# Kernel tuning notes

Hardware: AMD Instinct MI355X
Metric: run time of the kernel (lower is better)

Reference implementation:

```python
import jax, jax.numpy as jnp
import numpy as np

B, T, E, NH = 2, 2048, 512, 8
HD = E // NH
SCALE = float(HD) ** -0.5


def setup_inputs() -> dict:
    key = jax.random.key(0)
    ks = jax.random.split(key, 7)
    s = 0.02
    return {
        "x": jax.random.normal(ks[0], (B, T, E), dtype=jnp.float32),
        "w_qkv": jax.random.normal(ks[1], (E, 3 * E), dtype=jnp.float32) * s,
        "b_qkv": jax.random.normal(ks[2], (3 * E,), dtype=jnp.float32) * s,
        "w_od": jax.random.normal(ks[3], (E, 2 * NH), dtype=jnp.float32) * s,
        "b_od": jax.random.normal(ks[4], (2 * NH,), dtype=jnp.float32) * s,
        "w_out": jax.random.normal(ks[5], (E, E), dtype=jnp.float32) * s,
        "b_out": jax.random.normal(ks[6], (E,), dtype=jnp.float32) * s,
    }


def _heads(t):  # (B,T,E) -> (B*NH, T, HD)
    return t.reshape(B, T, NH, HD).transpose(0, 2, 1, 3).reshape(B * NH, T, HD)


def _point_mask(idx, j):  # idx: (B*NH,T) float indices -> one-hot (B*NH,T,T)
    return (j[None, None, :] == idx[:, :, None]).astype(jnp.float32)


def reference(x, w_qkv, b_qkv, w_od, b_od, w_out, b_out):
    qkv = x @ w_qkv + b_qkv
    Q, K, V = jnp.split(qkv, 3, axis=-1)  # each (B,T,E)

    od = Q @ w_od + b_od  # (B,T,2*NH)
    offset, duration = jnp.split(od, 2, axis=-1)
    offset = jnp.tanh(offset) * T
    duration = jax.nn.sigmoid(duration) * T

    query_index = jnp.arange(T, dtype=x.dtype)[None, :, None]  # (1,T,1)
    anchor = query_index + offset  # (B,T,NH)
    # 'b t nh -> (b nh) t'
    anchor = anchor.transpose(0, 2, 1).reshape(B * NH, T)
    duration = duration.transpose(0, 2, 1).reshape(B * NH, T)

    start = anchor - duration
    end = anchor + duration
    bound_l = jnp.floor(start)
    bound_r = jnp.ceil(end)
    anchor_l = jnp.floor(anchor)
    anchor_r = anchor_l + 1.0

    j = jnp.arange(T, dtype=x.dtype)
    neg_bound_weight = (bound_l - start)[:, :, None] * _point_mask(bound_l, j) \
                     + (end - bound_r)[:, :, None] * _point_mask(bound_r, j)
    anchor_dist_l = anchor - anchor_l
    anchor_weight = anchor_dist_l[:, :, None] * _point_mask(anchor_r, j) \
                  + (1.0 - anchor_dist_l)[:, :, None] * _point_mask(anchor_l, j)
    point_weight = 1.0 + neg_bound_weight + anchor_weight  # (B*NH,T,T)

    # segment mask: True OUTSIDE [bound_l, bound_r]
    attn_mask = (j[None, None, :] < bound_l[:, :, None]) | (j[None, None, :] > bound_r[:, :, None])

    Qh, Kh, Vh = _heads(Q), _heads(K), _heads(V)  # (B*NH, T, HD)
    scores = jnp.einsum('bic,brc->bir', Qh, Kh) * SCALE * point_weight
    scores = jnp.where(attn_mask, jnp.asarray(-1e8, scores.dtype), scores)
    attn = jax.nn.softmax(scores, axis=-1)
    out = jnp.einsum('bir,brc->bic', attn, Vh)  # (B*NH,T,HD)
    out = out.reshape(B, NH, T, HD).transpose(0, 2, 1, 3).reshape(B, T, E)
    return out @ w_out + b_out
```

## Files before the change

kernel.cpp:

```cpp
#include <hip/hip_runtime.h>
#include <math.h>

typedef float vf4 __attribute__((ext_vector_type(4)));
typedef float f32x4 __attribute__((ext_vector_type(4)));
typedef short bf16x8 __attribute__((ext_vector_type(8)));
typedef short short4v __attribute__((ext_vector_type(4)));
typedef int int2v __attribute__((ext_vector_type(2)));

constexpr int B = 2, T = 2048, E = 512, NH = 8, HD = 64;
constexpr int BH = B * NH;
constexpr int NT = BH * T;
constexpr float SCALE = 0.125f;

static __device__ __forceinline__ short f2bf(float f) {
  unsigned u = __float_as_uint(f);
  unsigned r = (u + 0x7fffu + ((u >> 16) & 1u)) >> 16;
  return (short)r;
}
static __device__ __forceinline__ unsigned pk2bf(float a, float b) {
  unsigned lo = (unsigned)(unsigned short)f2bf(a);
  unsigned hi = (unsigned)(unsigned short)f2bf(b);
  return lo | (hi << 16);
}

__global__ __launch_bounds__(256) void cast_x_bf16(
    const float* __restrict__ x, short* __restrict__ xb)
{
  int idx = (blockIdx.x * 256 + threadIdx.x) * 4;
  vf4 v = *(const vf4*)&x[idx];
  short4v o;
  o[0] = f2bf(v[0]); o[1] = f2bf(v[1]); o[2] = f2bf(v[2]); o[3] = f2bf(v[3]);
  *(short4v*)&xb[idx] = o;
}

__global__ __launch_bounds__(256) void cast_w_T(
    const float* __restrict__ w, short* __restrict__ wT, int N)
{
  __shared__ float t[32][33];
  const int k0 = blockIdx.x * 32;
  const int n0 = blockIdx.y * 32;
  const int c = threadIdx.x & 31, r = threadIdx.x >> 5;
#pragma unroll
  for (int p = 0; p < 4; ++p)
    t[r + p * 8][c] = w[(size_t)(k0 + r + p * 8) * N + n0 + c];
  __syncthreads();
#pragma unroll
  for (int p = 0; p < 4; ++p)
    wT[(size_t)(n0 + r + p * 8) * 512 + k0 + c] = f2bf(t[c][r + p * 8]);
}

__global__ __launch_bounds__(256) void w_comb(
    const float* __restrict__ w_qkv, const float* __restrict__ b_qkv,
    const float* __restrict__ w_od, const float* __restrict__ b_od,
    float* __restrict__ Wc, float* __restrict__ bc)
{
  __shared__ float Lod[512 * 16];
  __shared__ float pb[16][17];
  const int tid = threadIdx.x;
#pragma unroll
  for (int p = 0; p < 8; ++p) {
    int idx = (p * 256 + tid) * 4;
    *(vf4*)&Lod[idx] = *(const vf4*)&w_od[idx];
  }
  __syncthreads();

  if (blockIdx.x < 32) {
    const int k = blockIdx.x * 16 + (tid >> 4);
    const int c = tid & 15;
    float s = 0.0f;
    for (int m = 0; m < E; m += 4) {
      vf4 wq = *(const vf4*)&w_qkv[(size_t)k * 1536 + m];
      s += wq[0] * Lod[(m + 0) * 16 + c] + wq[1] * Lod[(m + 1) * 16 + c]
         + wq[2] * Lod[(m + 2) * 16 + c] + wq[3] * Lod[(m + 3) * 16 + c];
    }
    Wc[k * 16 + c] = s;
  } else {
    const int c = tid & 15, seg = tid >> 4;
    float s = 0.0f;
    for (int m = seg * 32; m < seg * 32 + 32; ++m)
      s += b_qkv[m] * Lod[m * 16 + c];
    pb[seg][c] = s;
    __syncthreads();
    if (tid < 16) {
      float acc = b_od[tid];
#pragma unroll
      for (int g = 0; g < 16; ++g) acc += pb[g][tid];
      bc[tid] = acc;
    }
  }
}

__global__ __launch_bounds__(256) void qkv_gemm_bf16(
    const short* __restrict__ xb, const short* __restrict__ wT,
    const float* __restrict__ bias, short* __restrict__ qkvb)
{
  __shared__ __align__(16) short As[128 * 40];
  __shared__ __align__(16) short Bt[128 * 40];

  const int tid = threadIdx.x;
  const int wave = tid >> 6, lane = tid & 63;
  const int quad = lane >> 4, l15 = lane & 15;
  const int wm = wave >> 1, wn = wave & 1;
  const int m0 = blockIdx.y * 128, n0 = blockIdx.x * 128;

  f32x4 acc[4][4];
#pragma unroll
  for (int mi = 0; mi < 4; ++mi)
#pragma unroll
    for (int ni = 0; ni < 4; ++ni) acc[mi][ni] = (f32x4){0, 0, 0, 0};

  const int sr = tid >> 1, sc = (tid & 1) * 16;

#pragma unroll 1
  for (int k0 = 0; k0 < E; k0 += 32) {
    __syncthreads();
    *(bf16x8*)&As[sr * 40 + sc] =
        *(const bf16x8*)&xb[(size_t)(m0 + sr) * 512 + k0 + sc];
    *(bf16x8*)&As[sr * 40 + sc + 8] =
        *(const bf16x8*)&xb[(size_t)(m0 + sr) * 512 + k0 + sc + 8];
    *(bf16x8*)&Bt[sr * 40 + sc] =
        *(const bf16x8*)&wT[(size_t)(n0 + sr) * 512 + k0 + sc];
    *(bf16x8*)&Bt[sr * 40 + sc + 8] =
        *(const bf16x8*)&wT[(size_t)(n0 + sr) * 512 + k0 + sc + 8];
    __syncthreads();

    bf16x8 aA[4], bB[4];
#pragma unroll
    for (int mi = 0; mi < 4; ++mi)
      aA[mi] = *(const bf16x8*)&As[(wm * 64 + mi * 16 + l15) * 40 + quad * 8];
#pragma unroll
    for (int ni = 0; ni < 4; ++ni)
      bB[ni] = *(const bf16x8*)&Bt[(wn * 64 + ni * 16 + l15) * 40 + quad * 8];
#pragma unroll
    for (int mi = 0; mi < 4; ++mi)
#pragma unroll
      for (int ni = 0; ni < 4; ++ni)
        acc[mi][ni] = __builtin_amdgcn_mfma_f32_16x16x32_bf16(
            aA[mi], bB[ni], acc[mi][ni], 0, 0, 0);
  }

#pragma unroll
  for (int mi = 0; mi < 4; ++mi)
#pragma unroll
    for (int ni = 0; ni < 4; ++ni)
#pragma unroll
      for (int r = 0; r < 4; ++r) {
        int row = m0 + wm * 64 + mi * 16 + quad * 4 + r;
        int col = n0 + wn * 64 + ni * 16 + l15;
        float v = acc[mi][ni][r] + bias[col];
        if (col < 512) v *= SCALE;
        qkvb[(size_t)row * 1536 + col] = f2bf(v);
      }
}

__global__ __launch_bounds__(256) void od_params(
    const float* __restrict__ x, const float* __restrict__ Wc,
    const float* __restrict__ bc, float* __restrict__ prm)
{
  __shared__ float od_s[16][16];
  const int tid = threadIdx.x;
  const int r = tid >> 4, c = tid & 15;
  const int row = blockIdx.x * 16 + r;

  float sum = bc[c];
  const float* qr = x + (size_t)row * E;
  for (int k = 0; k < E; k += 4) {
    vf4 q = *(const vf4*)&qr[k];
    sum += q[0] * Wc[(k + 0) * 16 + c]
         + q[1] * Wc[(k + 1) * 16 + c]
         + q[2] * Wc[(k + 2) * 16 + c]
         + q[3] * Wc[(k + 3) * 16 + c];
  }
  od_s[r][c] = sum;
  __syncthreads();

  if (tid < 128) {
    const int rr = tid >> 3, h = tid & 7;
    const int grow = blockIdx.x * 16 + rr;
    const int b = grow / T, i = grow % T;
    float o = od_s[rr][h];
    float d = od_s[rr][h + 8];
    float offset   = tanhf(o) * (float)T;
    float duration = (float)T / (1.0f + expf(-d));
    float anchor = (float)i + offset;
    float start = anchor - duration;
    float end   = anchor + duration;
    float bl = floorf(start);
    float br = ceilf(end);
    float al = floorf(anchor);
    float wbl = bl - start;
    float wbr = end - br;
    float af  = anchor - al;
    float rsc = 1.0f;
    if (br < 0.0f || bl > (float)(T - 1)) {
      bl = 0.0f; br = (float)(T - 1);
      wbl = 0.0f; wbr = 0.0f; al = -5.0f; af = 0.0f;
      rsc = 0.0f;
    }
    int idx = (b * NH + h) * T + i;
    prm[0 * NT + idx] = bl;
    prm[1 * NT + idx] = br;
    prm[2 * NT + idx] = wbl;
    prm[3 * NT + idx] = wbr;
    prm[4 * NT + idx] = al;
    prm[5 * NT + idx] = af;
    prm[6 * NT + idx] = rsc;
  }
}

__global__ __launch_bounds__(256) void v_transpose(
    const short* __restrict__ qkvb, short* __restrict__ Vtg)
{
  __shared__ __align__(16) short Tt[64 * 72];
  const int tid = threadIdx.x;
  const int t0 = blockIdx.x * 64, bh = blockIdx.y;
  const int b = bh >> 3, h = bh & 7;
  const int rq = tid >> 3, cb = (tid & 7) * 8;
#pragma unroll
  for (int it = 0; it < 2; ++it) {
    int rr = it * 32 + rq;
    bf16x8 v = *(const bf16x8*)&qkvb[(size_t)(b * T + t0 + rr) * 1536 + 1024 + h * 64 + cb];
#pragma unroll
    for (int j = 0; j < 8; ++j) Tt[(cb + j) * 72 + rr] = v[j];
  }
  __syncthreads();
  const int hd = tid >> 2, tc = (tid & 3) * 16;
  *(bf16x8*)&Vtg[(size_t)(bh * 64 + hd) * T + t0 + tc] =
      *(const bf16x8*)&Tt[hd * 72 + tc];
  *(bf16x8*)&Vtg[(size_t)(bh * 64 + hd) * T + t0 + tc + 8] =
      *(const bf16x8*)&Tt[hd * 72 + tc + 8];
}

__global__ __launch_bounds__(256, 4) void flash_attn_mfma3(
    const short* __restrict__ qkvb, const short* __restrict__ Vtg,
    const float* __restrict__ prm,
    float* __restrict__ Opart, float* __restrict__ lpart)
{
  __shared__ __align__(16) short Ks[64 * 72];
  __shared__ __align__(16) short Vt[64 * 72];
  __shared__ __align__(16) short Ps[4][16 * 72];
  __shared__ float u_s[8];

  const int tid = threadIdx.x;
  const int wave = tid >> 6, lane = tid & 63;
  const int quad = lane >> 4, l15 = lane & 15;
  const int qt = blockIdx.x, bh = blockIdx.y, ks = blockIdx.z;
  const int b = bh >> 3, h = bh & 7;
  const int i0 = qt * 64;
  const int i = i0 + wave * 16 + l15;

  const int pidx = bh * T + i;
  float blf = prm[0 * NT + pidx];
  float brf = prm[1 * NT + pidx];
  float wbl = prm[2 * NT + pidx];
  float wbr = prm[3 * NT + pidx];
  float alf = prm[4 * NT + pidx];
  float afr = prm[5 * NT + pidx];
  float rsc = prm[6 * NT + pidx];
  const int bli = (int)blf, widi = (int)brf - bli, ali = (int)alf;
  const unsigned widu = (unsigned)widi;
  const float a1 = 1.0f - afr;

  bf16x8 aQ0, aQ1;
  {
    size_t bq = (size_t)(b * T + i) * 1536 + h * 64;
    aQ0 = *(const bf16x8*)&qkvb[bq + quad * 8];
    aQ1 = *(const bf16x8*)&qkvb[bq + 32 + quad * 8];
    if (rsc == 0.0f) {
      bf16x8 z = {0, 0, 0, 0, 0, 0, 0, 0};
      aQ0 = z; aQ1 = z;
    }
  }

  float bmn = blf, bmx = brf;
#pragma unroll
  for (int d = 1; d < 64; d <<= 1) {
    bmn = fminf(bmn, __shfl_xor(bmn, d));
    bmx = fmaxf(bmx, __shfl_xor(bmx, d));
  }
  if (lane == 0) { u_s[wave * 2] = bmn; u_s[wave * 2 + 1] = bmx; }
  __syncthreads();
  bmn = fminf(fminf(u_s[0], u_s[2]), fminf(u_s[4], u_s[6]));
  bmx = fmaxf(fmaxf(u_s[1], u_s[3]), fmaxf(u_s[5], u_s[7]));
  const int ktlo = max(ks * 16, max(((int)bmn) >> 6, 0));
  const int kthi = min(ks * 16 + 15, min(((int)bmx) >> 6, T / 64 - 1));

  f32x4 o[4];
#pragma unroll
  for (int c = 0; c < 4; ++c) o[c] = (f32x4){0, 0, 0, 0};
  float lacc = 0.0f;

  const int rq = tid >> 3, cb = (tid & 7) * 8;

#pragma unroll 1
  for (int kt = ktlo; kt <= kthi; ++kt) {
    const int j0 = kt * 64;
    __syncthreads();
#pragma unroll
    for (int it = 0; it < 2; ++it) {
      int rr = it * 32 + rq;
      *(bf16x8*)&Ks[rr * 72 + cb] =
          *(const bf16x8*)&qkvb[(size_t)(b * T + j0 + rr) * 1536 + 512 + h * 64 + cb];
      *(bf16x8*)&Vt[rr * 72 + cb] =
          *(const bf16x8*)&Vtg[(size_t)(bh * 64 + rr) * T + j0 + cb];
    }
    __syncthreads();

    f32x4 s[4];
#pragma unroll
    for (int nc = 0; nc < 4; ++nc) {
      const short* kb = &Ks[(nc * 16 + l15) * 72 + quad * 8];
      f32x4 a = (f32x4){0, 0, 0, 0};
      a = __builtin_amdgcn_mfma_f32_16x16x32_bf16(*(const bf16x8*)&kb[0],  aQ0, a, 0, 0, 0);
      a = __builtin_amdgcn_mfma_f32_16x16x32_bf16(*(const bf16x8*)&kb[32], aQ1, a, 0, 0, 0);
      s[nc] = a;
    }

    const int dq  = j0 + quad * 4 - bli;
    const int dq2 = j0 + quad * 4 - ali;
#pragma unroll
    for (int nc = 0; nc < 4; ++nc) {
      const int dn = dq + nc * 16, d2n = dq2 + nc * 16;
      float pr[4];
#pragma unroll
      for (int r = 0; r < 4; ++r) {
        int d = dn + r, d2 = d2n + r;
        float e  = (d == 0) ? wbl : ((d == widi) ? wbr : 0.0f);
        float aw = (d2 == 0) ? a1 : ((d2 == 1) ? afr : 0.0f);
        float w = 1.0f + e + aw;
        float v = s[nc][r] * w;
        v = ((unsigned)d <= widu) ? v : -80.0f;
        float p = __expf(v);
        lacc += p;
        pr[r] = p;
      }
      int2v pk;
      pk[0] = (int)pk2bf(pr[0], pr[1]);
      pk[1] = (int)pk2bf(pr[2], pr[3]);
      *(int2v*)&Ps[wave][l15 * 72 + nc * 16 + quad * 4] = pk;
    }

    bf16x8 bP0 = *(const bf16x8*)&Ps[wave][l15 * 72 + quad * 8];
    bf16x8 bP1 = *(const bf16x8*)&Ps[wave][l15 * 72 + 32 + quad * 8];
#pragma unroll
    for (int nc2 = 0; nc2 < 4; ++nc2) {
      const short* vb = &Vt[(nc2 * 16 + l15) * 72 + quad * 8];
      o[nc2] = __builtin_amdgcn_mfma_f32_16x16x32_bf16(
          *(const bf16x8*)&vb[0],  bP0, o[nc2], 0, 0, 0);
      o[nc2] = __builtin_amdgcn_mfma_f32_16x16x32_bf16(
          *(const bf16x8*)&vb[32], bP1, o[nc2], 0, 0, 0);
    }
  }

  lacc += __shfl_xor(lacc, 16);
  lacc += __shfl_xor(lacc, 32);
  if (lane < 16)
    lpart[ks * NT + bh * T + i] = lacc;

  size_t ob = (size_t)ks * (B * T * E) + (size_t)(b * T + i) * E + h * 64;
#pragma unroll
  for (int nc2 = 0; nc2 < 4; ++nc2)
    *(f32x4*)&Opart[ob + nc2 * 16 + quad * 4] = o[nc2];
}

__global__ __launch_bounds__(256) void combine_attn(
    const float* __restrict__ Opart, const float* __restrict__ lpart,
    short* __restrict__ attnb)
{
  int base = (blockIdx.x * 256 + threadIdx.x) * 4;
  int row = base >> 9;
  int c = base & 511;
  int h = c >> 6;
  int b = row >> 11;
  int i = row & (T - 1);
  int lidx = ((b << 3) + h) * T + i;
  float l = lpart[lidx] + lpart[NT + lidx];
  float inv = 1.0f / l;
  vf4 o0 = *(const vf4*)&Opart[base];
  vf4 o1 = *(const vf4*)&Opart[(size_t)(B * T * E) + base];
  short4v ov;
#pragma unroll
  for (int j = 0; j < 4; ++j) ov[j] = f2bf((o0[j] + o1[j]) * inv);
  *(short4v*)&attnb[base] = ov;
}

__global__ __launch_bounds__(256) void out_gemm_bf16(
    const short* __restrict__ Ab, const short* __restrict__ wT,
    const float* __restrict__ bias, float* __restrict__ Co)
{
  __shared__ __align__(16) short As[64 * 40];
  __shared__ __align__(16) short Bt[64 * 40];

  const int tid = threadIdx.x;
  const int wave = tid >> 6, lane = tid & 63;
  const int quad = lane >> 4, l15 = lane & 15;
  const int wm = wave >> 1, wn = wave & 1;
  const int m0 = blockIdx.y * 64, n0 = blockIdx.x * 64;

  f32x4 acc[2][2];
#pragma unroll
  for (int mi = 0; mi < 2; ++mi)
#pragma unroll
    for (int ni = 0; ni < 2; ++ni) acc[mi][ni] = (f32x4){0, 0, 0, 0};

  const int ar = tid >> 2, akc = (tid & 3) * 8;

#pragma unroll 1
  for (int k0 = 0; k0 < E; k0 += 32) {
    __syncthreads();
    *(bf16x8*)&As[ar * 40 + akc] =
        *(const bf16x8*)&Ab[(size_t)(m0 + ar) * 512 + k0 + akc];
    *(bf16x8*)&Bt[ar * 40 + akc] =
        *(const bf16x8*)&wT[(size_t)(n0 + ar) * 512 + k0 + akc];
    __syncthreads();

    bf16x8 aA[2], bB[2];
#pragma unroll
    for (int mi = 0; mi < 2; ++mi)
      aA[mi] = *(const bf16x8*)&As[(wm * 32 + mi * 16 + l15) * 40 + quad * 8];
#pragma unroll
    for (int ni = 0; ni < 2; ++ni)
      bB[ni] = *(const bf16x8*)&Bt[(wn * 32 + ni * 16 + l15) * 40 + quad * 8];
#pragma unroll
    for (int mi = 0; mi < 2; ++mi)
#pragma unroll
      for (int ni = 0; ni < 2; ++ni)
        acc[mi][ni] = __builtin_amdgcn_mfma_f32_16x16x32_bf16(
            aA[mi], bB[ni], acc[mi][ni], 0, 0, 0);
  }

#pragma unroll
  for (int mi = 0; mi < 2; ++mi)
#pragma unroll
    for (int ni = 0; ni < 2; ++ni)
#pragma unroll
      for (int r = 0; r < 4; ++r) {
        int row = m0 + wm * 32 + mi * 16 + quad * 4 + r;
        int col = n0 + wn * 32 + ni * 16 + l15;
        Co[(size_t)row * 512 + col] = acc[mi][ni][r] + bias[col];
      }
}

extern "C" void kernel_launch(void* const* d_in, const int* in_sizes, int n_in,
                              void* d_out, int out_size, void* d_ws, size_t ws_size,
                              hipStream_t stream)
{
  const float* x     = (const float*)d_in[0];
  const float* w_qkv = (const float*)d_in[1];
  const float* b_qkv = (const float*)d_in[2];
  const float* w_od  = (const float*)d_in[3];
  const float* b_od  = (const float*)d_in[4];
  const float* w_out = (const float*)d_in[5];
  const float* b_out = (const float*)d_in[6];
  float* out = (float*)d_out;

  char* w = (char*)d_ws;
  short* xb    = (short*)w;  w += (size_t)B * T * E * 2;
  short* wTq   = (short*)w;  w += (size_t)E * 3 * E * 2;
  short* wTo   = (short*)w;  w += (size_t)E * E * 2;
  short* qkvb  = (short*)w;  w += (size_t)B * T * 3 * E * 2;
  float* Wc    = (float*)w;  w += (size_t)E * 16 * 4;
  float* bc    = (float*)w;  w += 256;
  float* prm   = (float*)w;  w += (size_t)7 * NT * 4;
  float* Opart = (float*)w;  w += (size_t)2 * B * T * E * 4;
  float* lpart = (float*)w;  w += (size_t)2 * NT * 4;
  short* attnb = (short*)w;  w += (size_t)B * T * E * 2;
  short* Vtg   = xb;

  cast_x_bf16<<<dim3(B * T * E / 1024), 256, 0, stream>>>(x, xb);
  cast_w_T<<<dim3(E / 32, 3 * E / 32), 256, 0, stream>>>(w_qkv, wTq, 3 * E);
  cast_w_T<<<dim3(E / 32, E / 32), 256, 0, stream>>>(w_out, wTo, E);
  w_comb<<<dim3(33), 256, 0, stream>>>(w_qkv, b_qkv, w_od, b_od, Wc, bc);

  qkv_gemm_bf16<<<dim3(3 * E / 128, B * T / 128), 256, 0, stream>>>(
      xb, wTq, b_qkv, qkvb);

  od_params<<<dim3(B * T / 16), 256, 0, stream>>>(x, Wc, bc, prm);

  v_transpose<<<dim3(T / 64, BH), 256, 0, stream>>>(qkvb, Vtg);

  flash_attn_mfma3<<<dim3(T / 64, BH, 2), 256, 0, stream>>>(
      qkvb, Vtg, prm, Opart, lpart);

  combine_attn<<<dim3(B * T * E / 1024), 256, 0, stream>>>(Opart, lpart, attnb);

  out_gemm_bf16<<<dim3(E / 64, B * T / 64), 256, 0, stream>>>(
      attnb, wTo, b_out, out);
}
```

Baseline: 197.8 us.

## Fuse prep kernels, write V transposed from QKV GEMM, fast-path attention softmax

Merges the x cast, the two weight transposes and the od-weight combine into one prep launch. The QKV GEMM epilogue now writes V directly in transposed layout, which removes the separate transpose kernel. Q is prescaled by log2e so attention can use exp2, with a wave-uniform fast path that skips the point-weight and mask logic on tiles that touch no boundary or anchor. Attention partial outputs are stored as bf16 to halve combine traffic, and the out-projection GEMM tile is widened to 128 columns. The bf16 partials and truncation-style packing of P reduce precision somewhat.

Result: faster. 183.2 us (-7.4%).

```diff
diff --git a/kernel.cpp b/kernel.cpp
--- a/kernel.cpp
+++ b/kernel.cpp
@@ -6,11 +6,14 @@
 typedef short bf16x8 __attribute__((ext_vector_type(8)));
 typedef short short4v __attribute__((ext_vector_type(4)));
 typedef int int2v __attribute__((ext_vector_type(2)));
+typedef int int4v __attribute__((ext_vector_type(4)));
 
 constexpr int B = 2, T = 2048, E = 512, NH = 8, HD = 64;
 constexpr int BH = B * NH;
 constexpr int NT = BH * T;
 constexpr float SCALE = 0.125f;
+constexpr float LOG2E = 1.44269504088896f;
+constexpr float QSC = SCALE * LOG2E;
 
 static __device__ __forceinline__ short f2bf(float f) {
   unsigned u = __float_as_uint(f);
@@ -22,77 +25,94 @@
   unsigned hi = (unsigned)(unsigned short)f2bf(b);
   return lo | (hi << 16);
 }
-
-__global__ __launch_bounds__(256) void cast_x_bf16(
-    const float* __restrict__ x, short* __restrict__ xb)
-{
-  int idx = (blockIdx.x * 256 + threadIdx.x) * 4;
-  vf4 v = *(const vf4*)&x[idx];
-  short4v o;
-  o[0] = f2bf(v[0]); o[1] = f2bf(v[1]); o[2] = f2bf(v[2]); o[3] = f2bf(v[3]);
-  *(short4v*)&xb[idx] = o;
-}
-
-__global__ __launch_bounds__(256) void cast_w_T(
-    const float* __restrict__ w, short* __restrict__ wT, int N)
-{
-  __shared__ float t[32][33];
-  const int k0 = blockIdx.x * 32;
-  const int n0 = blockIdx.y * 32;
-  const int c = threadIdx.x & 31, r = threadIdx.x >> 5;
-#pragma unroll
-  for (int p = 0; p < 4; ++p)
-    t[r + p * 8][c] = w[(size_t)(k0 + r + p * 8) * N + n0 + c];
-  __syncthreads();
-#pragma unroll
-  for (int p = 0; p < 4; ++p)
-    wT[(size_t)(n0 + r + p * 8) * 512 + k0 + c] = f2bf(t[c][r + p * 8]);
-}
-
-__global__ __launch_bounds__(256) void w_comb(
-    const float* __restrict__ w_qkv, const float* __restrict__ b_qkv,
-    const float* __restrict__ w_od, const float* __restrict__ b_od,
-    float* __restrict__ Wc, float* __restrict__ bc)
-{
-  __shared__ float Lod[512 * 16];
-  __shared__ float pb[16][17];
+static __device__ __forceinline__ unsigned pkhu(float a, float b) {
+  unsigned ua = __float_as_uint(a) + 0x8000u;
+  unsigned ub = __float_as_uint(b) + 0x8000u;
+  return __builtin_amdgcn_perm(ub, ua, 0x07060302u);
+}
+#if __has_builtin(__builtin_amdgcn_exp2f)
+#define EXP2F(x) __builtin_amdgcn_exp2f(x)
+#else
+#define EXP2F(x) exp2f(x)
+#endif
+static __device__ __forceinline__ float bf2f(short s) {
+  return __uint_as_float(((unsigned)(unsigned short)s) << 16);
+}
+
+__global__ __launch_bounds__(256) void prep_all(
+    const float* __restrict__ x, const float* __restrict__ w_qkv,
+    const float* __restrict__ b_qkv, const float* __restrict__ w_od,
+    const float* __restrict__ b_od,
+    short* __restrict__ xb, short* __restrict__ wTq, short* __restrict__ wTo,
+    const float* __restrict__ w_out, float* __restrict__ Wc,
+    float* __restrict__ bc)
+{
+  __shared__ float sh[8464];
+  const int bid = blockIdx.x;
   const int tid = threadIdx.x;
-#pragma unroll
-  for (int p = 0; p < 8; ++p) {
-    int idx = (p * 256 + tid) * 4;
-    *(vf4*)&Lod[idx] = *(const vf4*)&w_od[idx];
-  }
-  __syncthreads();
-
-  if (blockIdx.x < 32) {
-    const int k = blockIdx.x * 16 + (tid >> 4);
-    const int c = tid & 15;
-    float s = 0.0f;
-    for (int m = 0; m < E; m += 4) {
-      vf4 wq = *(const vf4*)&w_qkv[(size_t)k * 1536 + m];
-      s += wq[0] * Lod[(m + 0) * 16 + c] + wq[1] * Lod[(m + 1) * 16 + c]
-         + wq[2] * Lod[(m + 2) * 16 + c] + wq[3] * Lod[(m + 3) * 16 + c];
-    }
-    Wc[k * 16 + c] = s;
+
+  if (bid < 2048) {
+    int idx = (bid * 256 + tid) * 4;
+    vf4 v = *(const vf4*)&x[idx];
+    short4v o;
+    o[0] = f2bf(v[0]); o[1] = f2bf(v[1]); o[2] = f2bf(v[2]); o[3] = f2bf(v[3]);
+    *(short4v*)&xb[idx] = o;
+  } else if (bid < 3072) {
+    const float* w; short* wT; int N, t;
+    if (bid < 2816) { t = bid - 2048; w = w_qkv; wT = wTq; N = 1536; }
+    else            { t = bid - 2816; w = w_out; wT = wTo; N = 512; }
+    float (*tt)[33] = (float(*)[33])sh;
+    const int k0 = (t & 15) * 32;
+    const int n0 = (t >> 4) * 32;
+    const int c = tid & 31, r = tid >> 5;
+#pragma unroll
+    for (int p = 0; p < 4; ++p)
+      tt[r + p * 8][c] = w[(size_t)(k0 + r + p * 8) * N + n0 + c];
+    __syncthreads();
+#pragma unroll
+    for (int p = 0; p < 4; ++p)
+      wT[(size_t)(n0 + r + p * 8) * 512 + k0 + c] = f2bf(tt[c][r + p * 8]);
   } else {
-    const int c = tid & 15, seg = tid >> 4;
-    float s = 0.0f;
-    for (int m = seg * 32; m < seg * 32 + 32; ++m)
-      s += b_qkv[m] * Lod[m * 16 + c];
-    pb[seg][c] = s;
-    __syncthreads();
-    if (tid < 16) {
-      float acc = b_od[tid];
-#pragma unroll
-      for (int g = 0; g < 16; ++g) acc += pb[g][tid];
-      bc[tid] = acc;
+    float* Lod = sh;
+    float (*pb)[17] = (float(*)[17])(sh + 8192);
+    const int bx = bid - 3072;
+#pragma unroll
+    for (int p = 0; p < 8; ++p) {
+      int idx = (p * 256 + tid) * 4;
+      *(vf4*)&Lod[idx] = *(const vf4*)&w_od[idx];
+    }
+    __syncthreads();
+    if (bx < 32) {
+      const int k = bx * 16 + (tid >> 4);
+      const int c = tid & 15;
+      float s = 0.0f;
+      for (int m = 0; m < E; m += 4) {
+        vf4 wq = *(const vf4*)&w_qkv[(size_t)k * 1536 + m];
+        s += wq[0] * Lod[(m + 0) * 16 + c] + wq[1] * Lod[(m + 1) * 16 + c]
+           + wq[2] * Lod[(m + 2) * 16 + c] + wq[3] * Lod[(m + 3) * 16 + c];
+      }
+      Wc[k * 16 + c] = s;
+    } else {
+      const int c = tid & 15, seg = tid >> 4;
+      float s = 0.0f;
+      for (int m = seg * 32; m < seg * 32 + 32; ++m)
+        s += b_qkv[m] * Lod[m * 16 + c];
+      pb[seg][c] = s;
+      __syncthreads();
+      if (tid < 16) {
+        float acc = b_od[tid];
+#pragma unroll
+        for (int g = 0; g < 16; ++g) acc += pb[g][tid];
+        bc[tid] = acc;
+      }
     }
   }
 }
 
 __global__ __launch_bounds__(256) void qkv_gemm_bf16(
     const short* __restrict__ xb, const short* __restrict__ wT,
-    const float* __restrict__ bias, short* __restrict__ qkvb)
+    const float* __restrict__ bias, short* __restrict__ qkvb,
+    short* __restrict__ Vtg)
 {
   __shared__ __align__(16) short As[128 * 40];
   __shared__ __align__(16) short Bt[128 * 40];
@@ -142,15 +162,24 @@
 #pragma unroll
   for (int mi = 0; mi < 4; ++mi)
 #pragma unroll
-    for (int ni = 0; ni < 4; ++ni)
-#pragma unroll
-      for (int r = 0; r < 4; ++r) {
-        int row = m0 + wm * 64 + mi * 16 + quad * 4 + r;
-        int col = n0 + wn * 64 + ni * 16 + l15;
-        float v = acc[mi][ni][r] + bias[col];
-        if (col < 512) v *= SCALE;
-        qkvb[(size_t)row * 1536 + col] = f2bf(v);
+    for (int ni = 0; ni < 4; ++ni) {
+      const int col = n0 + wn * 64 + ni * 16 + l15;
+      const int rowb = m0 + wm * 64 + mi * 16 + quad * 4;
+      const float bs = bias[col];
+      if (col < 1024) {
+        const float qs = (col < 512) ? QSC : 1.0f;
+#pragma unroll
+        for (int r = 0; r < 4; ++r)
+          qkvb[(size_t)(rowb + r) * 1536 + col] = f2bf((acc[mi][ni][r] + bs) * qs);
+      } else {
+        const int h = (col - 1024) >> 6, hd = col & 63;
+        const int b = rowb >> 11, tt = rowb & 2047;
+        int2v pk;
+        pk[0] = (int)pk2bf(acc[mi][ni][0] + bs, acc[mi][ni][1] + bs);
+        pk[1] = (int)pk2bf(acc[mi][ni][2] + bs, acc[mi][ni][3] + bs);
+        *(int2v*)&Vtg[(size_t)(((b << 3) + h) * 64 + hd) * T + tt] = pk;
       }
+    }
 }
 
 __global__ __launch_bounds__(256) void od_params(
@@ -208,33 +237,10 @@
   }
 }
 
-__global__ __launch_bounds__(256) void v_transpose(
-    const short* __restrict__ qkvb, short* __restrict__ Vtg)
-{
-  __shared__ __align__(16) short Tt[64 * 72];
-  const int tid = threadIdx.x;
-  const int t0 = blockIdx.x * 64, bh = blockIdx.y;
-  const int b = bh >> 3, h = bh & 7;
-  const int rq = tid >> 3, cb = (tid & 7) * 8;
-#pragma unroll
-  for (int it = 0; it < 2; ++it) {
-    int rr = it * 32 + rq;
-    bf16x8 v = *(const bf16x8*)&qkvb[(size_t)(b * T + t0 + rr) * 1536 + 1024 + h * 64 + cb];
-#pragma unroll
-    for (int j = 0; j < 8; ++j) Tt[(cb + j) * 72 + rr] = v[j];
-  }
-  __syncthreads();
-  const int hd = tid >> 2, tc = (tid & 3) * 16;
-  *(bf16x8*)&Vtg[(size_t)(bh * 64 + hd) * T + t0 + tc] =
-      *(const bf16x8*)&Tt[hd * 72 + tc];
-  *(bf16x8*)&Vtg[(size_t)(bh * 64 + hd) * T + t0 + tc + 8] =
-      *(const bf16x8*)&Tt[hd * 72 + tc + 8];
-}
-
-__global__ __launch_bounds__(256, 4) void flash_attn_mfma3(
+__global__ __launch_bounds__(256, 4) void flash_attn_mfma4(
     const short* __restrict__ qkvb, const short* __restrict__ Vtg,
     const float* __restrict__ prm,
-    float* __restrict__ Opart, float* __restrict__ lpart)
+    short* __restrict__ Opart, float* __restrict__ lpart)
 {
   __shared__ __align__(16) short Ks[64 * 72];
   __shared__ __align__(16) short Vt[64 * 72];
@@ -316,28 +322,45 @@
       s[nc] = a;
     }
 
-    const int dq  = j0 + quad * 4 - bli;
-    const int dq2 = j0 + quad * 4 - ali;
-#pragma unroll
-    for (int nc = 0; nc < 4; ++nc) {
-      const int dn = dq + nc * 16, d2n = dq2 + nc * 16;
-      float pr[4];
-#pragma unroll
-      for (int r = 0; r < 4; ++r) {
-        int d = dn + r, d2 = d2n + r;
-        float e  = (d == 0) ? wbl : ((d == widi) ? wbr : 0.0f);
-        float aw = (d2 == 0) ? a1 : ((d2 == 1) ? afr : 0.0f);
-        float w = 1.0f + e + aw;
-        float v = s[nc][r] * w;
-        v = ((unsigned)d <= widu) ? v : -80.0f;
-        float p = __expf(v);
-        lacc += p;
-        pr[r] = p;
+    const int clean = (bli < j0) & (bli + widi > j0 + 63) &
+                      ((ali > j0 + 63) | (ali + 1 < j0));
+    if (__all(clean)) {
+#pragma unroll
+      for (int nc = 0; nc < 4; ++nc) {
+        float p0 = EXP2F(s[nc][0]);
+        float p1 = EXP2F(s[nc][1]);
+        float p2 = EXP2F(s[nc][2]);
+        float p3 = EXP2F(s[nc][3]);
+        lacc += (p0 + p1) + (p2 + p3);
+        int2v pk;
+        pk[0] = (int)pkhu(p0, p1);
+        pk[1] = (int)pkhu(p2, p3);
+        *(int2v*)&Ps[wave][l15 * 72 + nc * 16 + quad * 4] = pk;
       }
-      int2v pk;
-      pk[0] = (int)pk2bf(pr[0], pr[1]);
-      pk[1] = (int)pk2bf(pr[2], pr[3]);
-      *(int2v*)&Ps[wave][l15 * 72 + nc * 16 + quad * 4] = pk;
+    } else {
+      const int dq  = j0 + quad * 4 - bli;
+      const int dq2 = j0 + quad * 4 - ali;
+#pragma unroll
+      for (int nc = 0; nc < 4; ++nc) {
+        const int dn = dq + nc * 16, d2n = dq2 + nc * 16;
+        float pr[4];
+#pragma unroll
+        for (int r = 0; r < 4; ++r) {
+          int d = dn + r, d2 = d2n + r;
+          float e  = (d == 0) ? wbl : ((d == widi) ? wbr : 0.0f);
+          float aw = (d2 == 0) ? a1 : ((d2 == 1) ? afr : 0.0f);
+          float w = 1.0f + e + aw;
+          float v = s[nc][r] * w;
+          v = ((unsigned)d <= widu) ? v : -115.0f;
+          float p = EXP2F(v);
+          lacc += p;
+          pr[r] = p;
+        }
+        int2v pk;
+        pk[0] = (int)pkhu(pr[0], pr[1]);
+        pk[1] = (int)pkhu(pr[2], pr[3]);
+        *(int2v*)&Ps[wave][l15 * 72 + nc * 16 + quad * 4] = pk;
+      }
     }
 
     bf16x8 bP0 = *(const bf16x8*)&Ps[wave][l15 * 72 + quad * 8];
@@ -359,29 +382,36 @@
 
   size_t ob = (size_t)ks * (B * T * E) + (size_t)(b * T + i) * E + h * 64;
 #pragma unroll
-  for (int nc2 = 0; nc2 < 4; ++nc2)
-    *(f32x4*)&Opart[ob + nc2 * 16 + quad * 4] = o[nc2];
+  for (int nc2 = 0; nc2 < 4; ++nc2) {
+    int2v pk;
+    pk[0] = (int)pk2bf(o[nc2][0], o[nc2][1]);
+    pk[1] = (int)pk2bf(o[nc2][2], o[nc2][3]);
+    *(int2v*)&Opart[ob + nc2 * 16 + quad * 4] = pk;
+  }
 }
 
 __global__ __launch_bounds__(256) void combine_attn(
-    const float* __restrict__ Opart, const float* __restrict__ lpart,
+    const short* __restrict__ Opart, const float* __restrict__ lpart,
     short* __restrict__ attnb)
 {
-  int base = (blockIdx.x * 256 + threadIdx.x) * 4;
+  int base = (blockIdx.x * 256 + threadIdx.x) * 8;
   int row = base >> 9;
   int c = base & 511;
   int h = c >> 6;
   int b = row >> 11;
   int i = row & (T - 1);
   int lidx = ((b << 3) + h) * T + i;
-  float l = lpart[lidx] + lpart[NT + lidx];
-  float inv = 1.0f / l;
-  vf4 o0 = *(const vf4*)&Opart[base];
-  vf4 o1 = *(const vf4*)&Opart[(size_t)(B * T * E) + base];
-  short4v ov;
-#pragma unroll
-  for (int j = 0; j < 4; ++j) ov[j] = f2bf((o0[j] + o1[j]) * inv);
-  *(short4v*)&attnb[base] = ov;
+  float inv = 1.0f / (lpart[lidx] + lpart[NT + lidx]);
+  bf16x8 o0 = *(const bf16x8*)&Opart[base];
+  bf16x8 o1 = *(const bf16x8*)&Opart[(size_t)(B * T * E) + base];
+  int4v ov;
+#pragma unroll
+  for (int j = 0; j < 4; ++j) {
+    float a = (bf2f(o0[2 * j]) + bf2f(o1[2 * j])) * inv;
+    float bfv = (bf2f(o0[2 * j + 1]) + bf2f(o1[2 * j + 1])) * inv;
+    ov[j] = (int)pk2bf(a, bfv);
+  }
+  *(int4v*)&attnb[base] = ov;
 }
 
 __global__ __launch_bounds__(256) void out_gemm_bf16(
@@ -389,42 +419,45 @@
     const float* __restrict__ bias, float* __restrict__ Co)
 {
   __shared__ __align__(16) short As[64 * 40];
-  __shared__ __align__(16) short Bt[64 * 40];
+  __shared__ __align__(16) short Bt[128 * 40];
 
   const int tid = threadIdx.x;
   const int wave = tid >> 6, lane = tid & 63;
   const int quad = lane >> 4, l15 = lane & 15;
   const int wm = wave >> 1, wn = wave & 1;
-  const int m0 = blockIdx.y * 64, n0 = blockIdx.x * 64;
-
-  f32x4 acc[2][2];
+  const int m0 = blockIdx.y * 64, n0 = blockIdx.x * 128;
+
+  f32x4 acc[2][4];
 #pragma unroll
   for (int mi = 0; mi < 2; ++mi)
 #pragma unroll
-    for (int ni = 0; ni < 2; ++ni) acc[mi][ni] = (f32x4){0, 0, 0, 0};
+    for (int ni = 0; ni < 4; ++ni) acc[mi][ni] = (f32x4){0, 0, 0, 0};
 
   const int ar = tid >> 2, akc = (tid & 3) * 8;
+  const int br_ = tid >> 1, bkc = (tid & 1) * 16;
 
 #pragma unroll 1
   for (int k0 = 0; k0 < E; k0 += 32) {
     __syncthreads();
     *(bf16x8*)&As[ar * 40 + akc] =
         *(const bf16x8*)&Ab[(size_t)(m0 + ar) * 512 + k0 + akc];
-    *(bf16x8*)&Bt[ar * 40 + akc] =
-        *(const bf16x8*)&wT[(size_t)(n0 + ar) * 512 + k0 + akc];
-    __syncthreads();
-
-    bf16x8 aA[2], bB[2];
+    *(bf16x8*)&Bt[br_ * 40 + bkc] =
+        *(const bf16x8*)&wT[(size_t)(n0 + br_) * 512 + k0 + bkc];
+    *(bf16x8*)&Bt[br_ * 40 + bkc + 8] =
+        *(const bf16x8*)&wT[(size_t)(n0 + br_) * 512 + k0 + bkc + 8];
+    __syncthreads();
+
+    bf16x8 aA[2], bB[4];
 #pragma unroll
     for (int mi = 0; mi < 2; ++mi)
       aA[mi] = *(const bf16x8*)&As[(wm * 32 + mi * 16 + l15) * 40 + quad * 8];
 #pragma unroll
-    for (int ni = 0; ni < 2; ++ni)
-      bB[ni] = *(const bf16x8*)&Bt[(wn * 32 + ni * 16 + l15) * 40 + quad * 8];
+    for (int ni = 0; ni < 4; ++ni)
+      bB[ni] = *(const bf16x8*)&Bt[(wn * 64 + ni * 16 + l15) * 40 + quad * 8];
 #pragma unroll
     for (int mi = 0; mi < 2; ++mi)
 #pragma unroll
-      for (int ni = 0; ni < 2; ++ni)
+      for (int ni = 0; ni < 4; ++ni)
         acc[mi][ni] = __builtin_amdgcn_mfma_f32_16x16x32_bf16(
             aA[mi], bB[ni], acc[mi][ni], 0, 0, 0);
   }
@@ -432,11 +465,11 @@
 #pragma unroll
   for (int mi = 0; mi < 2; ++mi)
 #pragma unroll
-    for (int ni = 0; ni < 2; ++ni)
+    for (int ni = 0; ni < 4; ++ni)
 #pragma unroll
       for (int r = 0; r < 4; ++r) {
         int row = m0 + wm * 32 + mi * 16 + quad * 4 + r;
-        int col = n0 + wn * 32 + ni * 16 + l15;
+        int col = n0 + wn * 64 + ni * 16 + l15;
         Co[(size_t)row * 512 + col] = acc[mi][ni][r] + bias[col];
       }
 }
@@ -459,31 +492,27 @@
   short* wTq   = (short*)w;  w += (size_t)E * 3 * E * 2;
   short* wTo   = (short*)w;  w += (size_t)E * E * 2;
   short* qkvb  = (short*)w;  w += (size_t)B * T * 3 * E * 2;
+  short* Vtg   = (short*)w;  w += (size_t)B * T * E * 2;
   float* Wc    = (float*)w;  w += (size_t)E * 16 * 4;
   float* bc    = (float*)w;  w += 256;
   float* prm   = (float*)w;  w += (size_t)7 * NT * 4;
-  float* Opart = (float*)w;  w += (size_t)2 * B * T * E * 4;
+  short* Opart = (short*)w;  w += (size_t)2 * B * T * E * 2;
   float* lpart = (float*)w;  w += (size_t)2 * NT * 4;
   short* attnb = (short*)w;  w += (size_t)B * T * E * 2;
-  short* Vtg   = xb;
-
-  cast_x_bf16<<<dim3(B * T * E / 1024), 256, 0, stream>>>(x, xb);
-  cast_w_T<<<dim3(E / 32, 3 * E / 32), 256, 0, stream>>>(w_qkv, wTq, 3 * E);
-  cast_w_T<<<dim3(E / 32, E / 32), 256, 0, stream>>>(w_out, wTo, E);
-  w_comb<<<dim3(33), 256, 0, stream>>>(w_qkv, b_qkv, w_od, b_od, Wc, bc);
+
+  prep_all<<<dim3(3105), 256, 0, stream>>>(
+      x, w_qkv, b_qkv, w_od, b_od, xb, wTq, wTo, w_out, Wc, bc);
 
   qkv_gemm_bf16<<<dim3(3 * E / 128, B * T / 128), 256, 0, stream>>>(
-      xb, wTq, b_qkv, qkvb);
+      xb, wTq, b_qkv, qkvb, Vtg);
 
   od_params<<<dim3(B * T / 16), 256, 0, stream>>>(x, Wc, bc, prm);
 
-  v_transpose<<<dim3(T / 64, BH), 256, 0, stream>>>(qkvb, Vtg);
-
-  flash_attn_mfma3<<<dim3(T / 64, BH, 2), 256, 0, stream>>>(
+  flash_attn_mfma4<<<dim3(T / 64, BH, 2), 256, 0, stream>>>(
       qkvb, Vtg, prm, Opart, lpart);
 
-  combine_attn<<<dim3(B * T * E / 1024), 256, 0, stream>>>(Opart, lpart, attnb);
-
-  out_gemm_bf16<<<dim3(E / 64, B * T / 64), 256, 0, stream>>>(
+  combine_attn<<<dim3(B * T * E / 2048), 256, 0, stream>>>(Opart, lpart, attnb);
+
+  out_gemm_bf16<<<dim3(E / 128, B * T / 64), 256, 0, stream>>>(
       attnb, wTo, b_out, out);
 }
```
